# Optimization experiments

Measured on AMD Instinct MI355X. Metric: run time of the kernel, lower is better.

The kernel has to match this reference:

```python
import jax, jax.numpy as jnp
import numpy as np

GRAPH_SIZE = 512  # N: graph_size from init


def setup_inputs() -> dict:
    key = jax.random.key(0)
    k1, k2 = jax.random.split(key)
    B, N, C_IN, C_OUT = 128, GRAPH_SIZE, 128, 128
    # X packs [adjacency | features] along last dim, matching the torch forward
    X = jax.random.uniform(k1, (B, N, N + C_IN), dtype=jnp.float32)
    W = jax.random.normal(k2, (C_IN, C_OUT), dtype=jnp.float32)
    return {"X": X, "W": W}


def reference(X, W):
    N = GRAPH_SIZE
    A = X[:, :, :N]            # [B, N, N] dense adjacency
    feat = X[:, :, N:]         # [B, N, C_in]
    # D = diag(rowsum(A)); pinv(D).sqrt() == diag(1/sqrt(deg)) with 0 where deg==0
    deg = jnp.sum(A, axis=2)   # [B, N]
    d_inv_sqrt = jnp.where(deg > 0, 1.0 / jnp.sqrt(deg), 0.0)
    A_hat = A + jnp.eye(N, dtype=A.dtype)  # A + I
    # D^-1/2 @ A_hat @ D^-1/2 as elementwise row/col scaling (diag matmuls)
    A_norm = d_inv_sqrt[:, :, None] * A_hat * d_inv_sqrt[:, None, :]
    # relu(A_norm @ X @ W)
    h = jnp.einsum('bnm,bmf->bnf', A_norm, feat)
    out = jax.nn.relu(jnp.einsum('bnf,fo->bno', h, W))
    return jnp.concatenate([A, out], axis=2)  # [B, N, N + C_out]
```

## Files before the change

kernel.cpp:

```cpp
#include <hip/hip_runtime.h>
#include <stdint.h>

#define GS   512
#define CF   128
#define XROW 640
#define NB   128

typedef __attribute__((ext_vector_type(4))) float          f32x4;
typedef __attribute__((ext_vector_type(8))) short          s16x8;
typedef __attribute__((ext_vector_type(4))) unsigned short u16x4;

__device__ __forceinline__ unsigned short f2bf(float f) {
    unsigned u = __builtin_bit_cast(unsigned, f);
    u = (u + 0x7fffu + ((u >> 16) & 1u)) >> 16;
    return (unsigned short)u;
}
__device__ __forceinline__ float bf2f(unsigned short h) {
    unsigned u = ((unsigned)h) << 16;
    return __builtin_bit_cast(float, u);
}
__device__ __forceinline__ void glds16(const void* g, void* l) {
    __builtin_amdgcn_global_load_lds(
        (const __attribute__((address_space(1))) void*)g,
        (__attribute__((address_space(3))) void*)l, 16, 0, 0);
}

__global__ __launch_bounds__(256) void k1_deg_copy(const float* __restrict__ X,
                                                   float* __restrict__ out,
                                                   float* __restrict__ dis) {
    const int wv = threadIdx.x >> 6, l = threadIdx.x & 63;
    const int gr = (blockIdx.x << 2) + wv;
    const f32x4* rp = (const f32x4*)(X + (size_t)gr * XROW);
    f32x4* op = (f32x4*)(out + (size_t)gr * XROW);
    f32x4 v0 = rp[l], v1 = rp[l + 64];
    op[l] = v0; op[l + 64] = v1;
    float s = (v0[0] + v0[1]) + (v0[2] + v0[3]) + (v1[0] + v1[1]) + (v1[2] + v1[3]);
#pragma unroll
    for (int off = 32; off; off >>= 1) s += __shfl_xor(s, off, 64);
    if (l == 0) dis[gr] = (s > 0.f) ? (1.f / sqrtf(s)) : 0.f;
}

__global__ __launch_bounds__(256) void k2_featw(const float* __restrict__ X,
                                                const float* __restrict__ W,
                                                const float* __restrict__ dis,
                                                unsigned short* __restrict__ fwdT) {
    __shared__ __align__(16) float sf[64 * 128];
    __shared__ __align__(16) unsigned short swt[128 * 136];
    const int t = threadIdx.x, l = t & 63, wv = t >> 6;
    const int m0 = blockIdx.x << 6;
    const int b  = m0 >> 9;
    const int ml0 = m0 & (GS - 1);

    const char* fb = (const char*)(X + (size_t)m0 * XROW + GS);
    char* sfb = (char*)sf;
#pragma unroll
    for (int it = 0; it < 8; ++it) {
        int chunk = it * 256 + t;
        int row = chunk >> 5, c16 = chunk & 31;
        int c16s = c16 ^ (row & 7);
        glds16(fb + (size_t)row * (XROW * 4) + c16s * 16,
               sfb + it * 4096 + wv * 1024);
    }
    {
        int c = t >> 1, f0 = (t & 1) << 6;
        const float* wp = W + c * CF + f0;
#pragma unroll 8
        for (int j = 0; j < 64; ++j)
            swt[(f0 + j) * 136 + c] = f2bf(wp[j]);
    }
    __syncthreads();

    const int wr = wv >> 1, wc = wv & 1;
    const int lr = l & 15, lk = l >> 4;
    f32x4 acc[2][4];
#pragma unroll
    for (int i = 0; i < 2; ++i)
#pragma unroll
        for (int j = 0; j < 4; ++j)
#pragma unroll
            for (int r = 0; r < 4; ++r) acc[i][j][r] = 0.f;

#pragma unroll
    for (int ks = 0; ks < 4; ++ks) {
        s16x8 af[2];
#pragma unroll
        for (int i = 0; i < 2; ++i) {
            int row = (wr << 5) + (i << 4) + lr;
            int cb = (ks << 3) + (lk << 1);
            int c0 = cb ^ (row & 7), c1 = (cb + 1) ^ (row & 7);
            f32x4 x0 = *(const f32x4*)&sf[row * 128 + (c0 << 2)];
            f32x4 x1 = *(const f32x4*)&sf[row * 128 + (c1 << 2)];
            s16x8 a;
            a[0] = f2bf(x0[0]); a[1] = f2bf(x0[1]); a[2] = f2bf(x0[2]); a[3] = f2bf(x0[3]);
            a[4] = f2bf(x1[0]); a[5] = f2bf(x1[1]); a[6] = f2bf(x1[2]); a[7] = f2bf(x1[3]);
            af[i] = a;
        }
#pragma unroll
        for (int j = 0; j < 4; ++j) {
            int f = (wc << 6) + (j << 4) + lr;
            s16x8 bf = *(const s16x8*)&swt[f * 136 + (ks << 5) + (lk << 3)];
#pragma unroll
            for (int i = 0; i < 2; ++i)
                acc[i][j] = __builtin_amdgcn_mfma_f32_16x16x32_bf16(af[i], bf, acc[i][j], 0, 0, 0);
        }
    }

#pragma unroll
    for (int i = 0; i < 2; ++i) {
        int mr = (wr << 5) + (i << 4) + (lk << 2);
        f32x4 d4 = *(const f32x4*)&dis[m0 + mr];
#pragma unroll
        for (int j = 0; j < 4; ++j) {
            int f = (wc << 6) + (j << 4) + lr;
            u16x4 o;
            o[0] = f2bf(d4[0] * acc[i][j][0]);
            o[1] = f2bf(d4[1] * acc[i][j][1]);
            o[2] = f2bf(d4[2] * acc[i][j][2]);
            o[3] = f2bf(d4[3] * acc[i][j][3]);
            *(u16x4*)&fwdT[((size_t)(b * CF + f) << 9) + ml0 + mr] = o;
        }
    }
}

__global__ __launch_bounds__(256) void k3_gcn(const float* __restrict__ X,
                                              const float* __restrict__ dis,
                                              const unsigned short* __restrict__ fwdT,
                                              float* __restrict__ out) {
    __shared__ __align__(16) float sa[2][64 * 32];
    __shared__ __align__(16) unsigned short sb[2][128 * 32];
    const int t = threadIdx.x, l = t & 63, wv = t >> 6;
    const int b = blockIdx.x >> 3;
    const int bm0 = (blockIdx.x & 7) << 6;
    const char* Ab = (const char*)(X + ((size_t)b * GS + bm0) * XROW);
    const unsigned short* Bb = fwdT + ((size_t)(b * CF) << 9);

    const int wr = wv >> 1, wc = wv & 1;
    const int lr = l & 15, lk = l >> 4;

    auto stage = [&](int buf, int kt) {
#pragma unroll
        for (int it = 0; it < 2; ++it) {
            int chunk = it * 256 + t;
            int row = chunk >> 3, c16 = chunk & 7;
            int c16s = c16 ^ (row & 7);
            glds16(Ab + (size_t)row * (XROW * 4) + kt * 128 + c16s * 16,
                   (char*)sa[buf] + it * 4096 + wv * 1024);
        }
#pragma unroll
        for (int it = 0; it < 2; ++it) {
            int chunk = it * 256 + t;
            int f = chunk >> 2, c16 = chunk & 3;
            glds16((const char*)Bb + ((size_t)f << 10) + kt * 64 + c16 * 16,
                   (char*)sb[buf] + it * 4096 + wv * 1024);
        }
    };

    f32x4 acc[2][4];
#pragma unroll
    for (int i = 0; i < 2; ++i)
#pragma unroll
        for (int j = 0; j < 4; ++j)
#pragma unroll
            for (int r = 0; r < 4; ++r) acc[i][j][r] = 0.f;

    stage(0, 0);
    int cur = 0;
    for (int kt = 0; kt < 16; ++kt) {
        __syncthreads();
        if (kt < 15) stage(cur ^ 1, kt + 1);
        s16x8 af[2];
#pragma unroll
        for (int i = 0; i < 2; ++i) {
            int row = (wr << 5) + (i << 4) + lr;
            int cb = lk << 1;
            int c0 = cb ^ (row & 7), c1 = (cb + 1) ^ (row & 7);
            const float* rbase = &sa[cur][row << 5];
            f32x4 x0 = *(const f32x4*)(rbase + (c0 << 2));
            f32x4 x1 = *(const f32x4*)(rbase + (c1 << 2));
            s16x8 a;
            a[0] = f2bf(x0[0]); a[1] = f2bf(x0[1]); a[2] = f2bf(x0[2]); a[3] = f2bf(x0[3]);
            a[4] = f2bf(x1[0]); a[5] = f2bf(x1[1]); a[6] = f2bf(x1[2]); a[7] = f2bf(x1[3]);
            af[i] = a;
        }
#pragma unroll
        for (int j = 0; j < 4; ++j) {
            int f = (wc << 6) + (j << 4) + lr;
            s16x8 bf = *(const s16x8*)&sb[cur][(f << 5) + (lk << 3)];
#pragma unroll
            for (int i = 0; i < 2; ++i)
                acc[i][j] = __builtin_amdgcn_mfma_f32_16x16x32_bf16(af[i], bf, acc[i][j], 0, 0, 0);
        }
        cur ^= 1;
    }

#pragma unroll
    for (int i = 0; i < 2; ++i) {
        int nr = bm0 + (wr << 5) + (i << 4) + (lk << 2);
        f32x4 d4 = *(const f32x4*)&dis[(b << 9) + nr];
#pragma unroll
        for (int j = 0; j < 4; ++j) {
            int f = (wc << 6) + (j << 4) + lr;
            u16x4 fw = *(const u16x4*)&Bb[((size_t)f << 9) + nr];
#pragma unroll
            for (int r = 0; r < 4; ++r) {
                float v = d4[r] * (acc[i][j][r] + bf2f(fw[r]));
                out[(size_t)(b * GS + nr + r) * XROW + GS + f] = v > 0.f ? v : 0.f;
            }
        }
    }
}

extern "C" void kernel_launch(void* const* d_in, const int* in_sizes, int n_in,
                              void* d_out, int out_size, void* d_ws, size_t ws_size,
                              hipStream_t stream) {
    const float* X = (const float*)d_in[0];
    const float* W = (const float*)d_in[1];
    float* out = (float*)d_out;
    float* dis = (float*)d_ws;
    unsigned short* fwdT = (unsigned short*)((char*)d_ws + (size_t)NB * GS * 4);

    hipLaunchKernelGGL(k1_deg_copy, dim3(NB * GS / 4),  dim3(256), 0, stream, X, out, dis);
    hipLaunchKernelGGL(k2_featw,    dim3(NB * GS / 64), dim3(256), 0, stream, X, W, dis, fwdT);
    hipLaunchKernelGGL(k3_gcn,      dim3(NB * GS / 64), dim3(256), 0, stream, X, dis, fwdT, out);
}
```

Before: 346.6 us.

## Pre-pack adjacency to bf16 MFMA fragment layout and pre-transpose W

The copy/degree kernel now also writes the adjacency as bf16 in an MFMA-fragment-ordered layout, so the aggregation kernel loads A fragments straight from global memory into registers with no LDS staging or in-loop conversion. A small new kernel converts and reorders W to bf16 once, and the feature-transform kernel fills LDS from it with async global-to-LDS copies instead of a scalar transpose. The intermediate feature product is stored in a tiled layout that matches the new B-fragment loads, and each wave computes a 16x128 tile. In exchange, an extra 64 MB bf16 adjacency buffer is written and read, and there is one more kernel launch.

```diff
diff --git a/kernel.cpp b/kernel.cpp
--- a/kernel.cpp
+++ b/kernel.cpp
@@ -9,6 +9,7 @@
 typedef __attribute__((ext_vector_type(4))) float          f32x4;
 typedef __attribute__((ext_vector_type(8))) short          s16x8;
 typedef __attribute__((ext_vector_type(4))) unsigned short u16x4;
+typedef __attribute__((ext_vector_type(8))) unsigned short u16x8;
 
 __device__ __forceinline__ unsigned short f2bf(float f) {
     unsigned u = __builtin_bit_cast(unsigned, f);
@@ -25,31 +26,49 @@
         (__attribute__((address_space(3))) void*)l, 16, 0, 0);
 }
 
-__global__ __launch_bounds__(256) void k1_deg_copy(const float* __restrict__ X,
-                                                   float* __restrict__ out,
-                                                   float* __restrict__ dis) {
+__global__ __launch_bounds__(256) void k0_wt(const float* __restrict__ W,
+                                             unsigned short* __restrict__ WTst) {
+    const int e = blockIdx.x * 256 + threadIdx.x;
+    const int j = e & 7, f = (e >> 3) & 127, q = e >> 10;
+    const int c = (q >> 2) * 32 + (q & 3) * 8 + j;
+    WTst[e] = f2bf(W[c * CF + f]);
+}
+
+__global__ __launch_bounds__(256) void k1_pre(const float* __restrict__ X,
+                                              float* __restrict__ out,
+                                              float* __restrict__ dis,
+                                              unsigned short* __restrict__ Abf) {
     const int wv = threadIdx.x >> 6, l = threadIdx.x & 63;
-    const int gr = (blockIdx.x << 2) + wv;
-    const f32x4* rp = (const f32x4*)(X + (size_t)gr * XROW);
-    f32x4* op = (f32x4*)(out + (size_t)gr * XROW);
-    f32x4 v0 = rp[l], v1 = rp[l + 64];
-    op[l] = v0; op[l + 64] = v1;
-    float s = (v0[0] + v0[1]) + (v0[2] + v0[3]) + (v1[0] + v1[1]) + (v1[2] + v1[3]);
-#pragma unroll
-    for (int off = 32; off; off >>= 1) s += __shfl_xor(s, off, 64);
-    if (l == 0) dis[gr] = (s > 0.f) ? (1.f / sqrtf(s)) : 0.f;
+    const int gbase = blockIdx.x << 3;
+#pragma unroll
+    for (int p = 0; p < 2; ++p) {
+        const int gr = gbase + wv + (p << 2);
+        const f32x4* rp = (const f32x4*)(X + (size_t)gr * XROW);
+        f32x4* op = (f32x4*)(out + (size_t)gr * XROW);
+        f32x4 v0 = rp[2 * l], v1 = rp[2 * l + 1];
+        op[2 * l] = v0; op[2 * l + 1] = v1;
+        u16x8 o;
+        o[0] = f2bf(v0[0]); o[1] = f2bf(v0[1]); o[2] = f2bf(v0[2]); o[3] = f2bf(v0[3]);
+        o[4] = f2bf(v1[0]); o[5] = f2bf(v1[1]); o[6] = f2bf(v1[2]); o[7] = f2bf(v1[3]);
+        const int b = gr >> 9, n = gr & (GS - 1);
+        const int rt = n >> 4, lr = n & 15;
+        *(u16x8*)((char*)Abf + (((size_t)(b * 32 + rt)) << 14) + (l << 8) + (lr << 4)) = o;
+        float s = (v0[0] + v0[1]) + (v0[2] + v0[3]) + (v1[0] + v1[1]) + (v1[2] + v1[3]);
+#pragma unroll
+        for (int off = 32; off; off >>= 1) s += __shfl_xor(s, off, 64);
+        if (l == 0) dis[gr] = (s > 0.f) ? (1.f / sqrtf(s)) : 0.f;
+    }
 }
 
 __global__ __launch_bounds__(256) void k2_featw(const float* __restrict__ X,
-                                                const float* __restrict__ W,
+                                                const unsigned short* __restrict__ WTst,
                                                 const float* __restrict__ dis,
                                                 unsigned short* __restrict__ fwdT) {
     __shared__ __align__(16) float sf[64 * 128];
-    __shared__ __align__(16) unsigned short swt[128 * 136];
+    __shared__ __align__(16) unsigned short swt[16384];
     const int t = threadIdx.x, l = t & 63, wv = t >> 6;
     const int m0 = blockIdx.x << 6;
-    const int b  = m0 >> 9;
-    const int ml0 = m0 & (GS - 1);
+    const int b = m0 >> 9, ml0 = m0 & (GS - 1);
 
     const char* fb = (const char*)(X + (size_t)m0 * XROW + GS);
     char* sfb = (char*)sf;
@@ -58,20 +77,15 @@
         int chunk = it * 256 + t;
         int row = chunk >> 5, c16 = chunk & 31;
         int c16s = c16 ^ (row & 7);
-        glds16(fb + (size_t)row * (XROW * 4) + c16s * 16,
-               sfb + it * 4096 + wv * 1024);
-    }
-    {
-        int c = t >> 1, f0 = (t & 1) << 6;
-        const float* wp = W + c * CF + f0;
-#pragma unroll 8
-        for (int j = 0; j < 64; ++j)
-            swt[(f0 + j) * 136 + c] = f2bf(wp[j]);
-    }
+        glds16(fb + (size_t)row * (XROW * 4) + c16s * 16, sfb + it * 4096 + wv * 1024);
+    }
+#pragma unroll
+    for (int it = 0; it < 8; ++it)
+        glds16((const char*)WTst + it * 4096 + wv * 1024 + l * 16,
+               (char*)swt + it * 4096 + wv * 1024);
     __syncthreads();
 
-    const int wr = wv >> 1, wc = wv & 1;
-    const int lr = l & 15, lk = l >> 4;
+    const int wr = wv >> 1, wc = wv & 1, lr = l & 15, lk = l >> 4;
     f32x4 acc[2][4];
 #pragma unroll
     for (int i = 0; i < 2; ++i)
@@ -98,10 +112,10 @@
 #pragma unroll
         for (int j = 0; j < 4; ++j) {
             int f = (wc << 6) + (j << 4) + lr;
-            s16x8 bf = *(const s16x8*)&swt[f * 136 + (ks << 5) + (lk << 3)];
+            s16x8 bfr = *(const s16x8*)&swt[((((ks << 2) | lk) << 7) | f) << 3];
 #pragma unroll
             for (int i = 0; i < 2; ++i)
-                acc[i][j] = __builtin_amdgcn_mfma_f32_16x16x32_bf16(af[i], bf, acc[i][j], 0, 0, 0);
+                acc[i][j] = __builtin_amdgcn_mfma_f32_16x16x32_bf16(af[i], bfr, acc[i][j], 0, 0, 0);
         }
     }
 
@@ -109,6 +123,8 @@
     for (int i = 0; i < 2; ++i) {
         int mr = (wr << 5) + (i << 4) + (lk << 2);
         f32x4 d4 = *(const f32x4*)&dis[m0 + mr];
+        int mg = ml0 + mr;
+        int ktm = mg >> 5, q3 = (mg >> 3) & 3, jm = mg & 7;
 #pragma unroll
         for (int j = 0; j < 4; ++j) {
             int f = (wc << 6) + (j << 4) + lr;
@@ -117,95 +133,64 @@
             o[1] = f2bf(d4[1] * acc[i][j][1]);
             o[2] = f2bf(d4[2] * acc[i][j][2]);
             o[3] = f2bf(d4[3] * acc[i][j][3]);
-            *(u16x4*)&fwdT[((size_t)(b * CF + f) << 9) + ml0 + mr] = o;
-        }
-    }
-}
-
-__global__ __launch_bounds__(256) void k3_gcn(const float* __restrict__ X,
+            *(u16x4*)((char*)fwdT + ((size_t)b << 17) + (((ktm << 2) | q3) << 11)
+                      + (f << 4) + (jm << 1)) = o;
+        }
+    }
+}
+
+__global__ __launch_bounds__(256) void k3_gcn(const unsigned short* __restrict__ Abf,
                                               const float* __restrict__ dis,
                                               const unsigned short* __restrict__ fwdT,
                                               float* __restrict__ out) {
-    __shared__ __align__(16) float sa[2][64 * 32];
-    __shared__ __align__(16) unsigned short sb[2][128 * 32];
-    const int t = threadIdx.x, l = t & 63, wv = t >> 6;
-    const int b = blockIdx.x >> 3;
-    const int bm0 = (blockIdx.x & 7) << 6;
-    const char* Ab = (const char*)(X + ((size_t)b * GS + bm0) * XROW);
-    const unsigned short* Bb = fwdT + ((size_t)(b * CF) << 9);
-
-    const int wr = wv >> 1, wc = wv & 1;
-    const int lr = l & 15, lk = l >> 4;
+    __shared__ __align__(16) unsigned short sb[2][4096];
+    const int t = threadIdx.x, l = t & 63, wv = t >> 6, lr = l & 15, lk = l >> 4;
+    const int b = blockIdx.x >> 3, bm0 = (blockIdx.x & 7) << 6;
+    const char* Bt = (const char*)fwdT + ((size_t)b << 17);
+    const int rt = (bm0 >> 4) + wv;
+    const char* Ab = (const char*)Abf + (((size_t)(b * 32 + rt)) << 14);
 
     auto stage = [&](int buf, int kt) {
 #pragma unroll
-        for (int it = 0; it < 2; ++it) {
-            int chunk = it * 256 + t;
-            int row = chunk >> 3, c16 = chunk & 7;
-            int c16s = c16 ^ (row & 7);
-            glds16(Ab + (size_t)row * (XROW * 4) + kt * 128 + c16s * 16,
-                   (char*)sa[buf] + it * 4096 + wv * 1024);
-        }
-#pragma unroll
-        for (int it = 0; it < 2; ++it) {
-            int chunk = it * 256 + t;
-            int f = chunk >> 2, c16 = chunk & 3;
-            glds16((const char*)Bb + ((size_t)f << 10) + kt * 64 + c16 * 16,
+        for (int it = 0; it < 2; ++it)
+            glds16(Bt + (kt << 13) + it * 4096 + wv * 1024 + l * 16,
                    (char*)sb[buf] + it * 4096 + wv * 1024);
-        }
     };
 
-    f32x4 acc[2][4];
-#pragma unroll
-    for (int i = 0; i < 2; ++i)
-#pragma unroll
-        for (int j = 0; j < 4; ++j)
-#pragma unroll
-            for (int r = 0; r < 4; ++r) acc[i][j][r] = 0.f;
+    f32x4 acc[8];
+#pragma unroll
+    for (int j = 0; j < 8; ++j)
+#pragma unroll
+        for (int r = 0; r < 4; ++r) acc[j][r] = 0.f;
 
     stage(0, 0);
+    s16x8 a = *(const s16x8*)(Ab + (l << 4));
     int cur = 0;
     for (int kt = 0; kt < 16; ++kt) {
         __syncthreads();
         if (kt < 15) stage(cur ^ 1, kt + 1);
-        s16x8 af[2];
-#pragma unroll
-        for (int i = 0; i < 2; ++i) {
-            int row = (wr << 5) + (i << 4) + lr;
-            int cb = lk << 1;
-            int c0 = cb ^ (row & 7), c1 = (cb + 1) ^ (row & 7);
-            const float* rbase = &sa[cur][row << 5];
-            f32x4 x0 = *(const f32x4*)(rbase + (c0 << 2));
-            f32x4 x1 = *(const f32x4*)(rbase + (c1 << 2));
-            s16x8 a;
-            a[0] = f2bf(x0[0]); a[1] = f2bf(x0[1]); a[2] = f2bf(x0[2]); a[3] = f2bf(x0[3]);
-            a[4] = f2bf(x1[0]); a[5] = f2bf(x1[1]); a[6] = f2bf(x1[2]); a[7] = f2bf(x1[3]);
-            af[i] = a;
-        }
-#pragma unroll
-        for (int j = 0; j < 4; ++j) {
-            int f = (wc << 6) + (j << 4) + lr;
-            s16x8 bf = *(const s16x8*)&sb[cur][(f << 5) + (lk << 3)];
-#pragma unroll
-            for (int i = 0; i < 2; ++i)
-                acc[i][j] = __builtin_amdgcn_mfma_f32_16x16x32_bf16(af[i], bf, acc[i][j], 0, 0, 0);
-        }
-        cur ^= 1;
-    }
-
-#pragma unroll
-    for (int i = 0; i < 2; ++i) {
-        int nr = bm0 + (wr << 5) + (i << 4) + (lk << 2);
-        f32x4 d4 = *(const f32x4*)&dis[(b << 9) + nr];
-#pragma unroll
-        for (int j = 0; j < 4; ++j) {
-            int f = (wc << 6) + (j << 4) + lr;
-            u16x4 fw = *(const u16x4*)&Bb[((size_t)f << 9) + nr];
-#pragma unroll
-            for (int r = 0; r < 4; ++r) {
-                float v = d4[r] * (acc[i][j][r] + bf2f(fw[r]));
-                out[(size_t)(b * GS + nr + r) * XROW + GS + f] = v > 0.f ? v : 0.f;
-            }
+        s16x8 an = a;
+        if (kt < 15) an = *(const s16x8*)(Ab + ((kt + 1) << 10) + (l << 4));
+#pragma unroll
+        for (int j = 0; j < 8; ++j) {
+            s16x8 bfr = *(const s16x8*)&sb[cur][(lk << 10) + (j << 7) + (lr << 3)];
+            acc[j] = __builtin_amdgcn_mfma_f32_16x16x32_bf16(a, bfr, acc[j], 0, 0, 0);
+        }
+        a = an; cur ^= 1;
+    }
+
+    const int n0 = bm0 + (wv << 4) + (lk << 2);
+    f32x4 d4 = *(const f32x4*)&dis[(b << 9) + n0];
+    const int ktm = n0 >> 5, q3 = (n0 >> 3) & 3, jm = n0 & 7;
+#pragma unroll
+    for (int j = 0; j < 8; ++j) {
+        int f = (j << 4) + lr;
+        u16x4 fw = *(const u16x4*)(Bt + (((ktm << 2) | q3) << 11) + (f << 4) + (jm << 1));
+        float* ob = out + ((size_t)(b * GS + n0)) * XROW + GS + f;
+#pragma unroll
+        for (int r = 0; r < 4; ++r) {
+            float v = d4[r] * (acc[j][r] + bf2f(fw[r]));
+            ob[(size_t)r * XROW] = v > 0.f ? v : 0.f;
         }
     }
 }
@@ -216,10 +201,13 @@
     const float* X = (const float*)d_in[0];
     const float* W = (const float*)d_in[1];
     float* out = (float*)d_out;
-    float* dis = (float*)d_ws;
-    unsigned short* fwdT = (unsigned short*)((char*)d_ws + (size_t)NB * GS * 4);
-
-    hipLaunchKernelGGL(k1_deg_copy, dim3(NB * GS / 4),  dim3(256), 0, stream, X, out, dis);
-    hipLaunchKernelGGL(k2_featw,    dim3(NB * GS / 64), dim3(256), 0, stream, X, W, dis, fwdT);
-    hipLaunchKernelGGL(k3_gcn,      dim3(NB * GS / 64), dim3(256), 0, stream, X, dis, fwdT, out);
-}
+    float*          dis  = (float*)d_ws;
+    unsigned short* WTst = (unsigned short*)((char*)d_ws + 262144);
+    unsigned short* fwdT = (unsigned short*)((char*)d_ws + 294912);
+    unsigned short* Abf  = (unsigned short*)((char*)d_ws + 17072128);
+
+    hipLaunchKernelGGL(k0_wt,   dim3(64),   dim3(256), 0, stream, W, WTst);
+    hipLaunchKernelGGL(k1_pre,  dim3(NB * GS / 8),  dim3(256), 0, stream, X, out, dis, Abf);
+    hipLaunchKernelGGL(k2_featw, dim3(NB * GS / 64), dim3(256), 0, stream, X, WTst, dis, fwdT);
+    hipLaunchKernelGGL(k3_gcn,  dim3(NB * GS / 64), dim3(256), 0, stream, Abf, dis, fwdT, out);
+}
```

Measured after the change: 357.3 us. +3.1%, slower.
